# Performance work log

Measured on AMD Instinct MI355X. Metric: run time of the kernel, lower is better.

## Reference

```python
import jax, jax.numpy as jnp
import numpy as np

VOCAB, HIDDEN = 32000, 512
BATCH, SEQLEN = 256, 128


def setup_inputs() -> dict:
    key = jax.random.key(0)
    k1, k2, k3, k4, k5 = jax.random.split(key, 5)
    bound = 1.0 / np.sqrt(HIDDEN)  # PyTorch RNNCell init scale
    return {
        "input": jax.random.randint(k1, (BATCH, SEQLEN), 0, VOCAB, dtype=jnp.int64),
        "hidden": jnp.zeros((BATCH, HIDDEN), dtype=jnp.float32),
        "emb_table": jax.random.normal(k2, (VOCAB, HIDDEN), dtype=jnp.float32),
        "W_ih": jax.random.uniform(k3, (HIDDEN, HIDDEN), jnp.float32, -bound, bound),
        "W_hh": jax.random.uniform(k4, (HIDDEN, HIDDEN), jnp.float32, -bound, bound),
        "b_ih": jax.random.uniform(k5, (HIDDEN,), jnp.float32, -bound, bound),
        "b_hh": jax.random.uniform(jax.random.fold_in(key, 9), (HIDDEN,), jnp.float32, -bound, bound),
    }


def reference(input, hidden, emb_table, W_ih, W_hh, b_ih, b_hh):
    # embedded: [B, T, H]
    embedded = emb_table[input]
    # Precompute the input projection for all timesteps in one GEMM: [B, T, H]
    x_proj = jnp.einsum("bth,ih->bti", embedded, W_ih) + b_ih

    def step(h, x_t):
        # PyTorch RNNCell: h' = tanh(x W_ih^T + b_ih + h W_hh^T + b_hh)
        h_new = jnp.tanh(x_t + h @ W_hh.T + b_hh)
        return h_new, h_new

    h_final, outs = jax.lax.scan(step, hidden, jnp.swapaxes(x_proj, 0, 1))
    outputs = jnp.swapaxes(outs, 0, 1)  # [B, T, H]
    return outputs, h_final
```

## Files before the change

kernel.cpp:

```cpp
#include <hip/hip_runtime.h>
#include <cstdint>

#define VOCAB   32000
#define HIDDEN  512
#define BATCH   256
#define SEQLEN  128

typedef _Float16 f16;
typedef _Float16 f16x2 __attribute__((ext_vector_type(2)));
typedef _Float16 f16x4 __attribute__((ext_vector_type(4)));
typedef _Float16 f16x8 __attribute__((ext_vector_type(8)));
typedef float    f32x4 __attribute__((ext_vector_type(4)));


__global__ __launch_bounds__(256) void conv_f16_kernel(
    const float* __restrict__ emb, const float* __restrict__ wih,
    const float* __restrict__ whh, f16* __restrict__ emb16,
    f16* __restrict__ wih16, f16* __restrict__ whh16)
{
  const long long EMB_N = (long long)VOCAB * HIDDEN;
  const long long W_N   = (long long)HIDDEN * HIDDEN;
  long long idx = ((long long)blockIdx.x * blockDim.x + threadIdx.x) * 4;
  const float* src; f16* dst; long long off;
  if (idx < EMB_N)            { src = emb; dst = emb16; off = idx; }
  else if (idx < EMB_N + W_N) { src = wih; dst = wih16; off = idx - EMB_N; }
  else                        { src = whh; dst = whh16; off = idx - EMB_N - W_N; }
  float4 v = *(const float4*)(src + off);
  f16x4 o = { (f16)v.x, (f16)v.y, (f16)v.z, (f16)v.w };
  *(f16x4*)(dst + off) = o;
}

__global__ __launch_bounds__(256) void xproj_kernel(
    const int*   __restrict__ tokens,
    const f16*   __restrict__ emb16,
    const f16*   __restrict__ wih16,
    const float* __restrict__ b_ih,
    float*       __restrict__ out)
{
  const int lane = threadIdx.x & 63;
  const int wave = threadIdx.x >> 6;
  const int m0 = blockIdx.y * 128 + (wave >> 1) * 64;
  const int n0 = blockIdx.x * 128 + (wave & 1) * 64;
  const int lr = lane & 15;
  const int lg = lane >> 4;

  const f16* aptr[4];
  const f16* bptr[4];
#pragma unroll
  for (int mi = 0; mi < 4; ++mi) {
    int row = m0 + mi * 16 + lr;
    int tok = tokens[row];
    aptr[mi] = emb16 + (long long)tok * HIDDEN;
  }
#pragma unroll
  for (int ni = 0; ni < 4; ++ni) {
    int col = n0 + ni * 16 + lr;
    bptr[ni] = wih16 + (long long)col * HIDDEN;
  }

  f32x4 acc[4][4];
#pragma unroll
  for (int ni = 0; ni < 4; ++ni) {
    float b = b_ih[n0 + ni * 16 + lr];
#pragma unroll
    for (int mi = 0; mi < 4; ++mi) acc[mi][ni] = (f32x4){b, b, b, b};
  }

  for (int kt = 0; kt < 16; ++kt) {
    const int kb = kt * 32 + lg * 8;
    f16x8 af[4], bf[4];
#pragma unroll
    for (int mi = 0; mi < 4; ++mi) af[mi] = *(const f16x8*)(aptr[mi] + kb);
#pragma unroll
    for (int ni = 0; ni < 4; ++ni) bf[ni] = *(const f16x8*)(bptr[ni] + kb);
#pragma unroll
    for (int mi = 0; mi < 4; ++mi)
#pragma unroll
      for (int ni = 0; ni < 4; ++ni)
        acc[mi][ni] = __builtin_amdgcn_mfma_f32_16x16x32_f16(
            af[mi], bf[ni], acc[mi][ni], 0, 0, 0);
  }

#pragma unroll
  for (int mi = 0; mi < 4; ++mi)
#pragma unroll
    for (int ni = 0; ni < 4; ++ni)
#pragma unroll
      for (int j = 0; j < 4; ++j) {
        int rg = m0 + mi * 16 + lg * 4 + j;
        int cg = n0 + ni * 16 + lr;
        out[(long long)rg * HIDDEN + cg] = acc[mi][ni][j];
      }
}

__device__ __forceinline__ float dp2(uint32_t w, uint32_t h, float acc) {
  f16x2 wv = __builtin_bit_cast(f16x2, w);
  f16x2 hv = __builtin_bit_cast(f16x2, h);
#if __has_builtin(__builtin_amdgcn_fdot2)
  return __builtin_amdgcn_fdot2(wv, hv, acc, false);
#else
  acc = fmaf((float)wv.x, (float)hv.x, acc);
  acc = fmaf((float)wv.y, (float)hv.y, acc);
  return acc;
#endif
}

__global__ __launch_bounds__(1024, 4) void rnn_kernel(
    const f16*   __restrict__ whh16,
    const float* __restrict__ b_hh,
    const float* __restrict__ h0,
    float*       __restrict__ out,
    float*       __restrict__ hfin)
{
  extern __shared__ char smem[];
  uint4* hh4  = (uint4*)smem;
  float* pacc = (float*)(smem + 1024);
  uint4* ldsW = (uint4*)(smem + 1024 + 16384);

  const int tid = threadIdx.x;
  const int w   = tid >> 6;
  const int l   = tid & 63;
  const int s   = w >> 1;
  const int ib  = (w & 1) * 64 + l;
  const int b   = blockIdx.x;

  uint32_t wreg[96];
#pragma unroll
  for (int o = 0; o < 3; ++o) {
    const uint4* wr = (const uint4*)(whh16 + ((long long)(ib + o * 128) * HIDDEN + s * 64));
#pragma unroll
    for (int c = 0; c < 8; ++c) {
      uint4 v = wr[c];
      wreg[o * 32 + c * 4 + 0] = v.x; wreg[o * 32 + c * 4 + 1] = v.y;
      wreg[o * 32 + c * 4 + 2] = v.z; wreg[o * 32 + c * 4 + 3] = v.w;
    }
  }
  {
    const uint4* wr3 = (const uint4*)(whh16 + ((long long)(ib + 384) * HIDDEN + s * 64));
#pragma unroll
    for (int c = 0; c < 8; ++c) ldsW[c * 1024 + tid] = wr3[c];
  }

  if (tid < 512) ((f16*)hh4)[tid] = (f16)h0[(long long)b * HIDDEN + tid];
  const float bh = (tid < 512) ? b_hh[tid] : 0.f;
  float* xprow = out + (long long)b * SEQLEN * HIDDEN;
  float xpn = (tid < 512) ? xprow[tid] : 0.f;
  __syncthreads();

  for (int t = 0; t < SEQLEN; ++t) {
    const float xpv = xpn;
    const int tn = (t < SEQLEN - 1) ? t + 1 : t;
    if (tid < 512) xpn = xprow[tn * HIDDEN + tid];

    float a0 = 0.f, a1 = 0.f, a2 = 0.f, a3 = 0.f;
#pragma unroll
    for (int hc = 0; hc < 8; ++hc) {
      uint4 hv = hh4[s * 8 + hc];
      uint4 w3 = ldsW[hc * 1024 + tid];
      a0 = dp2(wreg[0 * 32 + hc * 4 + 0], hv.x, a0);
      a0 = dp2(wreg[0 * 32 + hc * 4 + 1], hv.y, a0);
      a0 = dp2(wreg[0 * 32 + hc * 4 + 2], hv.z, a0);
      a0 = dp2(wreg[0 * 32 + hc * 4 + 3], hv.w, a0);
      a1 = dp2(wreg[1 * 32 + hc * 4 + 0], hv.x, a1);
      a1 = dp2(wreg[1 * 32 + hc * 4 + 1], hv.y, a1);
      a1 = dp2(wreg[1 * 32 + hc * 4 + 2], hv.z, a1);
      a1 = dp2(wreg[1 * 32 + hc * 4 + 3], hv.w, a1);
      a2 = dp2(wreg[2 * 32 + hc * 4 + 0], hv.x, a2);
      a2 = dp2(wreg[2 * 32 + hc * 4 + 1], hv.y, a2);
      a2 = dp2(wreg[2 * 32 + hc * 4 + 2], hv.z, a2);
      a2 = dp2(wreg[2 * 32 + hc * 4 + 3], hv.w, a2);
      a3 = dp2(w3.x, hv.x, a3);
      a3 = dp2(w3.y, hv.y, a3);
      a3 = dp2(w3.z, hv.z, a3);
      a3 = dp2(w3.w, hv.w, a3);
    }
    pacc[s * 512 + ib]       = a0;
    pacc[s * 512 + ib + 128] = a1;
    pacc[s * 512 + ib + 256] = a2;
    pacc[s * 512 + ib + 384] = a3;
    __syncthreads();

    if (tid < 512) {
      float pre = xpv + bh;
#pragma unroll
      for (int s2 = 0; s2 < 8; ++s2) pre += pacc[s2 * 512 + tid];
      float h = tanhf(pre);
      xprow[t * HIDDEN + tid] = h;
      ((f16*)hh4)[tid] = (f16)h;
      if (t == SEQLEN - 1) hfin[(long long)b * HIDDEN + tid] = h;
    }
    __syncthreads();
  }
}

extern "C" void kernel_launch(void* const* d_in, const int* in_sizes, int n_in,
                              void* d_out, int out_size, void* d_ws, size_t ws_size,
                              hipStream_t stream) {
  const int*   tokens = (const int*)  d_in[0];
  const float* hidden = (const float*)d_in[1];
  const float* emb    = (const float*)d_in[2];
  const float* wih    = (const float*)d_in[3];
  const float* whh    = (const float*)d_in[4];
  const float* bih    = (const float*)d_in[5];
  const float* bhh    = (const float*)d_in[6];
  float* out = (float*)d_out;

  f16* emb16 = (f16*)d_ws;
  f16* wih16 = (f16*)((char*)d_ws + 32768000);
  f16* whh16 = (f16*)((char*)d_ws + 33292288);

  conv_f16_kernel<<<16512, 256, 0, stream>>>(emb, wih, whh, emb16, wih16, whh16);

  xproj_kernel<<<dim3(4, 256), 256, 0, stream>>>(tokens, emb16, wih16, bih, out);

  const int LDSB = 1024 + 16384 + 131072;
  hipFuncSetAttribute((const void*)rnn_kernel,
                      hipFuncAttributeMaxDynamicSharedMemorySize, LDSB);
  rnn_kernel<<<BATCH, 1024, LDSB, stream>>>(
      whh16, bhh, hidden, out, out + (long long)BATCH * SEQLEN * HIDDEN);
}
```

Baseline: 399.2 us.

## Halve RNN block to 512 threads with more register-resident W_hh slices

```diff
diff --git a/kernel.cpp b/kernel.cpp
--- a/kernel.cpp
+++ b/kernel.cpp
@@ -105,7 +105,7 @@
 #endif
 }
 
-__global__ __launch_bounds__(1024, 4) void rnn_kernel(
+__global__ __launch_bounds__(512, 2) void rnn_kernel(
     const f16*   __restrict__ whh16,
     const float* __restrict__ b_hh,
     const float* __restrict__ h0,
@@ -115,7 +115,7 @@
   extern __shared__ char smem[];
   uint4* hh4  = (uint4*)smem;
   float* pacc = (float*)(smem + 1024);
-  uint4* ldsW = (uint4*)(smem + 1024 + 16384);
+  uint4* ldsW = (uint4*)(smem + 1024 + 8192);
 
   const int tid = threadIdx.x;
   const int w   = tid >> 6;
@@ -124,55 +124,68 @@
   const int ib  = (w & 1) * 64 + l;
   const int b   = blockIdx.x;
 
-  uint32_t wreg[96];
+  uint32_t wreg[224];
 #pragma unroll
   for (int o = 0; o < 3; ++o) {
-    const uint4* wr = (const uint4*)(whh16 + ((long long)(ib + o * 128) * HIDDEN + s * 64));
+    const uint4* wr = (const uint4*)(whh16 + (ib + o * 128) * HIDDEN + s * 128);
+#pragma unroll
+    for (int c = 0; c < 16; ++c) {
+      uint4 v = wr[c];
+      wreg[o * 64 + c * 4 + 0] = v.x; wreg[o * 64 + c * 4 + 1] = v.y;
+      wreg[o * 64 + c * 4 + 2] = v.z; wreg[o * 64 + c * 4 + 3] = v.w;
+    }
+  }
+  {
+    const uint4* wr3 = (const uint4*)(whh16 + (ib + 384) * HIDDEN + s * 128);
 #pragma unroll
     for (int c = 0; c < 8; ++c) {
-      uint4 v = wr[c];
-      wreg[o * 32 + c * 4 + 0] = v.x; wreg[o * 32 + c * 4 + 1] = v.y;
-      wreg[o * 32 + c * 4 + 2] = v.z; wreg[o * 32 + c * 4 + 3] = v.w;
+      uint4 v = wr3[c];
+      wreg[192 + c * 4 + 0] = v.x; wreg[192 + c * 4 + 1] = v.y;
+      wreg[192 + c * 4 + 2] = v.z; wreg[192 + c * 4 + 3] = v.w;
     }
-  }
-  {
-    const uint4* wr3 = (const uint4*)(whh16 + ((long long)(ib + 384) * HIDDEN + s * 64));
-#pragma unroll
-    for (int c = 0; c < 8; ++c) ldsW[c * 1024 + tid] = wr3[c];
-  }
-
-  if (tid < 512) ((f16*)hh4)[tid] = (f16)h0[(long long)b * HIDDEN + tid];
-  const float bh = (tid < 512) ? b_hh[tid] : 0.f;
+#pragma unroll
+    for (int c = 0; c < 8; ++c) ldsW[c * 512 + tid] = wr3[8 + c];
+  }
+
+  ((f16*)hh4)[tid] = (f16)h0[(long long)b * HIDDEN + tid];
+  const float bh = b_hh[tid];
   float* xprow = out + (long long)b * SEQLEN * HIDDEN;
-  float xpn = (tid < 512) ? xprow[tid] : 0.f;
+  float xpn = xprow[tid];
   __syncthreads();
 
   for (int t = 0; t < SEQLEN; ++t) {
     const float xpv = xpn;
     const int tn = (t < SEQLEN - 1) ? t + 1 : t;
-    if (tid < 512) xpn = xprow[tn * HIDDEN + tid];
+    xpn = xprow[tn * HIDDEN + tid];
 
     float a0 = 0.f, a1 = 0.f, a2 = 0.f, a3 = 0.f;
 #pragma unroll
-    for (int hc = 0; hc < 8; ++hc) {
-      uint4 hv = hh4[s * 8 + hc];
-      uint4 w3 = ldsW[hc * 1024 + tid];
-      a0 = dp2(wreg[0 * 32 + hc * 4 + 0], hv.x, a0);
-      a0 = dp2(wreg[0 * 32 + hc * 4 + 1], hv.y, a0);
-      a0 = dp2(wreg[0 * 32 + hc * 4 + 2], hv.z, a0);
-      a0 = dp2(wreg[0 * 32 + hc * 4 + 3], hv.w, a0);
-      a1 = dp2(wreg[1 * 32 + hc * 4 + 0], hv.x, a1);
-      a1 = dp2(wreg[1 * 32 + hc * 4 + 1], hv.y, a1);
-      a1 = dp2(wreg[1 * 32 + hc * 4 + 2], hv.z, a1);
-      a1 = dp2(wreg[1 * 32 + hc * 4 + 3], hv.w, a1);
-      a2 = dp2(wreg[2 * 32 + hc * 4 + 0], hv.x, a2);
-      a2 = dp2(wreg[2 * 32 + hc * 4 + 1], hv.y, a2);
-      a2 = dp2(wreg[2 * 32 + hc * 4 + 2], hv.z, a2);
-      a2 = dp2(wreg[2 * 32 + hc * 4 + 3], hv.w, a2);
-      a3 = dp2(w3.x, hv.x, a3);
-      a3 = dp2(w3.y, hv.y, a3);
-      a3 = dp2(w3.z, hv.z, a3);
-      a3 = dp2(w3.w, hv.w, a3);
+    for (int hc = 0; hc < 16; ++hc) {
+      uint4 hv = hh4[s * 16 + hc];
+      a0 = dp2(wreg[hc * 4 + 0], hv.x, a0);
+      a0 = dp2(wreg[hc * 4 + 1], hv.y, a0);
+      a0 = dp2(wreg[hc * 4 + 2], hv.z, a0);
+      a0 = dp2(wreg[hc * 4 + 3], hv.w, a0);
+      a1 = dp2(wreg[64 + hc * 4 + 0], hv.x, a1);
+      a1 = dp2(wreg[64 + hc * 4 + 1], hv.y, a1);
+      a1 = dp2(wreg[64 + hc * 4 + 2], hv.z, a1);
+      a1 = dp2(wreg[64 + hc * 4 + 3], hv.w, a1);
+      a2 = dp2(wreg[128 + hc * 4 + 0], hv.x, a2);
+      a2 = dp2(wreg[128 + hc * 4 + 1], hv.y, a2);
+      a2 = dp2(wreg[128 + hc * 4 + 2], hv.z, a2);
+      a2 = dp2(wreg[128 + hc * 4 + 3], hv.w, a2);
+      if (hc < 8) {
+        a3 = dp2(wreg[192 + hc * 4 + 0], hv.x, a3);
+        a3 = dp2(wreg[192 + hc * 4 + 1], hv.y, a3);
+        a3 = dp2(wreg[192 + hc * 4 + 2], hv.z, a3);
+        a3 = dp2(wreg[192 + hc * 4 + 3], hv.w, a3);
+      } else {
+        uint4 wv = ldsW[(hc - 8) * 512 + tid];
+        a3 = dp2(wv.x, hv.x, a3);
+        a3 = dp2(wv.y, hv.y, a3);
+        a3 = dp2(wv.z, hv.z, a3);
+        a3 = dp2(wv.w, hv.w, a3);
+      }
     }
     pacc[s * 512 + ib]       = a0;
     pacc[s * 512 + ib + 128] = a1;
@@ -180,15 +193,12 @@
     pacc[s * 512 + ib + 384] = a3;
     __syncthreads();
 
-    if (tid < 512) {
-      float pre = xpv + bh;
-#pragma unroll
-      for (int s2 = 0; s2 < 8; ++s2) pre += pacc[s2 * 512 + tid];
-      float h = tanhf(pre);
-      xprow[t * HIDDEN + tid] = h;
-      ((f16*)hh4)[tid] = (f16)h;
-      if (t == SEQLEN - 1) hfin[(long long)b * HIDDEN + tid] = h;
-    }
+    float pre = xpv + bh +
+        ((pacc[tid] + pacc[512 + tid]) + (pacc[1024 + tid] + pacc[1536 + tid]));
+    float h = tanhf(pre);
+    xprow[t * HIDDEN + tid] = h;
+    ((f16*)hh4)[tid] = (f16)h;
+    if (t == SEQLEN - 1) hfin[(long long)b * HIDDEN + tid] = h;
     __syncthreads();
   }
 }
@@ -213,9 +223,9 @@
 
   xproj_kernel<<<dim3(4, 256), 256, 0, stream>>>(tokens, emb16, wih16, bih, out);
 
-  const int LDSB = 1024 + 16384 + 131072;
+  const int LDSB = 1024 + 8192 + 65536;
   hipFuncSetAttribute((const void*)rnn_kernel,
                       hipFuncAttributeMaxDynamicSharedMemorySize, LDSB);
-  rnn_kernel<<<BATCH, 1024, LDSB, stream>>>(
+  rnn_kernel<<<BATCH, 512, LDSB, stream>>>(
       whh16, bhh, hidden, out, out + (long long)BATCH * SEQLEN * HIDDEN);
 }
```

Measured after the change: 412.2 us. +3.2%, slower.
